# Performance work log

Measured on AMD Instinct MI355X. Metric: run time of the kernel, lower is better.

The kernel has to match this reference:

```python
import jax, jax.numpy as jnp
import numpy as np

R = 16
LORA_ALPHA = 32
SCALING = LORA_ALPHA / R  # use_rslora=False -> alpha/r = 2.0


def fwht(x):
    """Normalized fast Walsh-Hadamard transform along last axis (power-of-2 dim)."""
    n = x.shape[-1]
    batch = x.shape[:-1]
    h = 1
    while h < n:  # static loop, log2(n) iterations
        x = x.reshape(*batch, n // (2 * h), 2, h)
        a = x[..., 0, :]
        b = x[..., 1, :]
        x = jnp.stack([a + b, a - b], axis=-2).reshape(*batch, n)
        h *= 2
    return x * np.float32(1.0 / np.sqrt(n))


def quant_int8_ste(x):
    """Simulated symmetric per-row int8 quantization with straight-through estimator."""
    s = jnp.max(jnp.abs(x), axis=-1, keepdims=True) * np.float32(1.0 / 127.0)
    s = jnp.maximum(s, np.float32(1e-8))
    q = jnp.clip(jnp.round(x / s), -127.0, 127.0) * s
    return x + jax.lax.stop_gradient(q - x)


def setup_inputs() -> dict:
    key = jax.random.key(0)
    k1, k2, k3, k4 = jax.random.split(key, 4)
    B, S, D_in, D_out = 4, 2048, 4096, 4096
    x = jax.random.normal(k1, (B, S, D_in), dtype=jnp.float32)
    weight = jax.random.normal(k2, (D_out, D_in), dtype=jnp.float32) * np.float32(0.02)
    lora_A = jax.random.normal(k3, (R, D_in), dtype=jnp.float32) * np.float32(0.02)
    lora_B = jax.random.normal(k4, (D_out, R), dtype=jnp.float32) * np.float32(0.02)
    return {"x": x, "weight": weight, "lora_A": lora_A, "lora_B": lora_B}


def reference(x, weight, lora_A, lora_B):
    B, S, D_in = x.shape
    x2 = x.reshape(-1, D_in)  # [B*S, D_in]
    # Hadamard-rotate + quantize both operands (rotation is orthogonal, so
    # (xH)(WH)^T == xW^T up to quantization error) then GEMM.
    xq = quant_int8_ste(fwht(x2))          # [B*S, D_in]
    wq = quant_int8_ste(fwht(weight))      # [D_out, D_in]
    out = xq @ wq.T                        # [B*S, D_out]
    # LoRA side path (dropout p=0): B(A x) * scaling
    lora = (x2 @ lora_A.T) @ lora_B.T * np.float32(SCALING)
    return (out + lora).reshape(B, S, -1)
```

## Files before the change

### kernel.cpp

```cpp
#include <hip/hip_runtime.h>
#include <stdint.h>

typedef int v4i __attribute__((ext_vector_type(4)));

#define GLD_LDS16(gp, lp)                                                              \
  __builtin_amdgcn_global_load_lds((const __attribute__((address_space(1))) void*)(gp), \
                                   (__attribute__((address_space(3))) void*)(lp), 16, 0, 0)

__device__ __forceinline__ v4i lds_read_b128(uint32_t off) {
  v4i r;
  asm volatile("ds_read_b128 %0, %1" : "=v"(r) : "v"(off));
  return r;
}

__device__ __forceinline__ void fwht16(float v[16]) {
#pragma unroll
  for (int h = 1; h < 16; h <<= 1) {
#pragma unroll
    for (int i = 0; i < 16; ++i) {
      if (!(i & h)) {
        float a = v[i], b = v[i | h];
        v[i] = a + b;
        v[i | h] = a - b;
      }
    }
  }
}

__device__ __forceinline__ void fwht_row_load(const float* __restrict__ xr, int t,
                                              float v[16]) {
  const float4* p = reinterpret_cast<const float4*>(xr) + t * 4;
  float4 a = p[0], b = p[1], c = p[2], d = p[3];
  v[0] = a.x; v[1] = a.y; v[2] = a.z; v[3] = a.w;
  v[4] = b.x; v[5] = b.y; v[6] = b.z; v[7] = b.w;
  v[8] = c.x; v[9] = c.y; v[10] = c.z; v[11] = c.w;
  v[12] = d.x; v[13] = d.y; v[14] = d.z; v[15] = d.w;
}

__device__ __forceinline__ void fwht4096(float v[16], float* lds, int t) {
  fwht16(v);
#pragma unroll
  for (int e = 0; e < 16; ++e) {
    int idx = t * 16 + e;
    lds[idx + (idx >> 5)] = v[e];
  }
  __syncthreads();
#pragma unroll
  for (int e = 0; e < 16; ++e) {
    int idx = ((t >> 4) << 8) + (e << 4) + (t & 15);
    v[e] = lds[idx + (idx >> 5)];
  }
  fwht16(v);
#pragma unroll
  for (int e = 0; e < 16; ++e) {
    int idx = ((t >> 4) << 8) + (e << 4) + (t & 15);
    lds[idx + (idx >> 5)] = v[e];
  }
  __syncthreads();
#pragma unroll
  for (int e = 0; e < 16; ++e) {
    int idx = (e << 8) + t;
    v[e] = lds[idx + (idx >> 5)];
  }
  fwht16(v);
#pragma unroll
  for (int e = 0; e < 16; ++e) v[e] *= 0.015625f;
}

__global__ __launch_bounds__(256) void fwht_quant_kernel(const float* __restrict__ X,
                                                         int8_t* __restrict__ Q,
                                                         float* __restrict__ S) {
  const int row = blockIdx.x;
  const int t = threadIdx.x;
  __shared__ float lds[4224];
  __shared__ float wred[4];

  float v[16];
  fwht_row_load(X + (size_t)row * 4096, t, v);
  fwht4096(v, lds, t);

  float m = 0.f;
#pragma unroll
  for (int e = 0; e < 16; ++e) m = fmaxf(m, fabsf(v[e]));
#pragma unroll
  for (int off = 32; off > 0; off >>= 1) m = fmaxf(m, __shfl_xor(m, off));
  if ((t & 63) == 0) wred[t >> 6] = m;
  __syncthreads();
  m = fmaxf(fmaxf(wred[0], wred[1]), fmaxf(wred[2], wred[3]));
  const float s = fmaxf(m * (1.0f / 127.0f), 1e-8f);
  if (t == 0) S[row] = s;
  int8_t* qr = Q + (size_t)row * 4096;
#pragma unroll
  for (int e = 0; e < 16; ++e) {
    float q = rintf(v[e] / s);
    q = fminf(fmaxf(q, -127.f), 127.f);
    qr[(e << 8) + t] = (int8_t)(int)q;
  }
}

__global__ __launch_bounds__(256) void fwht_nq_kernel(const float* __restrict__ X,
                                                      float* __restrict__ F) {
  const int row = blockIdx.x;
  const int t = threadIdx.x;
  __shared__ float lds[4224];
  float v[16];
  fwht_row_load(X + (size_t)row * 4096, t, v);
  fwht4096(v, lds, t);
  float* fr = F + (size_t)row * 4096;
#pragma unroll
  for (int e = 0; e < 16; ++e) fr[(e << 8) + t] = v[e];
}

__global__ __launch_bounds__(256) void lora_t_partial_q(const int8_t* __restrict__ Qx,
                                                        const float* __restrict__ Sx,
                                                        const float* __restrict__ Ah,
                                                        float* __restrict__ tpart) {
  __shared__ float As[16][512];
  const int t = threadIdx.x;
  const int kc = blockIdx.y;
  const int row = blockIdx.x * 256 + t;
  for (int i = t; i < 2048; i += 256) {
    int r = i >> 7, c4 = i & 127;
    reinterpret_cast<float4*>(&As[r][0])[c4] =
        reinterpret_cast<const float4*>(Ah + (size_t)r * 4096 + kc * 512)[c4];
  }
  __syncthreads();
  float acc[16];
#pragma unroll
  for (int r = 0; r < 16; ++r) acc[r] = 0.f;
  const int8_t* xr = Qx + (size_t)row * 4096 + kc * 512;
  for (int k = 0; k < 512; k += 16) {
    int4 pv = *reinterpret_cast<const int4*>(xr + k);
    int us[4] = {pv.x, pv.y, pv.z, pv.w};
#pragma unroll
    for (int b = 0; b < 4; ++b) {
#pragma unroll
      for (int j = 0; j < 4; ++j) {
        float f = (float)((int)(int8_t)(us[b] >> (8 * j)));
        int kk = k + b * 4 + j;
#pragma unroll
        for (int r = 0; r < 16; ++r) acc[r] = fmaf(f, As[r][kk], acc[r]);
      }
    }
  }
  const float s = Sx[row];
  float* tp = tpart + ((size_t)kc * 8192 + row) * 16;
#pragma unroll
  for (int r = 0; r < 16; ++r) tp[r] = acc[r] * s;
}

__global__ __launch_bounds__(256) void lora_t_reduce_kernel(const float* __restrict__ tpart,
                                                            float* __restrict__ tmat) {
  int i = blockIdx.x * 256 + threadIdx.x;
  float s = 0.f;
#pragma unroll
  for (int kc = 0; kc < 8; ++kc) s += tpart[(size_t)kc * 131072 + i];
  tmat[i] = s;
}

__global__ __launch_bounds__(512, 2) void gemm_i8_kernel(
    const int8_t* __restrict__ Aq, const int8_t* __restrict__ Bq,
    const float* __restrict__ Sx, const float* __restrict__ Sw,
    const float* __restrict__ Tm, const float* __restrict__ LB,
    float* __restrict__ out) {
  __shared__ __align__(16) char smem[131072];

  const int tid = threadIdx.x;
  const int lane = tid & 63;
  const int w = tid >> 6;
  const int wm = w >> 2;
  const int wn = w & 3;

  int bid = (int)blockIdx.x;
  bid = (bid & 7) * 64 + (bid >> 3);
  const int bm = bid >> 4;
  const int bn = bid & 15;

  const int8_t* Ag = Aq + (size_t)bm * 256 * 4096;
  const int8_t* Bg = Bq + (size_t)bn * 256 * 4096;

  const uint32_t sbase = (uint32_t)(uintptr_t)(void*)smem;

  const size_t gA0 = (size_t)(w * 32 + (lane >> 2)) * 4096 +
                     (((lane & 3) ^ ((lane >> 3) & 3)) << 4);
  const size_t gA1 = gA0 + 16 * 4096;

#define STAGE_STEP(s)                                                   \
  do {                                                                  \
    char* dst = smem + ((s) & 3) * 32768 + w * 2048;                    \
    const size_t kb = (size_t)(s) << 6;                                 \
    GLD_LDS16(Ag + gA0 + kb, dst);                                      \
    GLD_LDS16(Ag + gA1 + kb, dst + 1024);                               \
    GLD_LDS16(Bg + gA0 + kb, dst + 16384);                              \
    GLD_LDS16(Bg + gA1 + kb, dst + 16384 + 1024);                       \
  } while (0)

  int aoff[8], boff[4];
#pragma unroll
  for (int mi = 0; mi < 8; ++mi) {
    int r = wm * 128 + mi * 16 + (lane & 15);
    aoff[mi] = r * 64 + ((((lane >> 4)) ^ ((r >> 1) & 3)) << 4);
  }
#pragma unroll
  for (int ni = 0; ni < 4; ++ni) {
    int r = wn * 64 + ni * 16 + (lane & 15);
    boff[ni] = 16384 + r * 64 + ((((lane >> 4)) ^ ((r >> 1) & 3)) << 4);
  }

  v4i acc[8][4];
#pragma unroll
  for (int i = 0; i < 8; ++i)
#pragma unroll
    for (int n = 0; n < 4; ++n) {
      v4i z = {0, 0, 0, 0};
      acc[i][n] = z;
    }

  STAGE_STEP(0);
  STAGE_STEP(1);
  STAGE_STEP(2);
  asm volatile("s_waitcnt vmcnt(8)" ::: "memory");
  __builtin_amdgcn_s_barrier();
  __builtin_amdgcn_sched_barrier(0);

#define MFMA16(MH)                                                                        \
  do {                                                                                    \
    __builtin_amdgcn_s_setprio(1);                                                        \
    _Pragma("unroll") for (int i = 0; i < 4; ++i) _Pragma("unroll") for (int n = 0;       \
                                                                        n < 4; ++n)       \
        acc[(MH)*4 + i][n] =                                                              \
        __builtin_amdgcn_mfma_i32_16x16x64_i8(af[i], bf[n], acc[(MH)*4 + i][n], 0, 0, 0); \
    __builtin_amdgcn_s_setprio(0);                                                        \
  } while (0)

#pragma unroll 1
  for (int t = 0; t < 64; ++t) {
    const uint32_t bufR = sbase + (t & 3) * 32768;
    if (t <= 60) STAGE_STEP(t + 3);

    v4i af[4], bf[4], af2[4];
#pragma unroll
    for (int n = 0; n < 4; ++n) bf[n] = lds_read_b128(bufR + boff[n]);
#pragma unroll
    for (int i = 0; i < 4; ++i) af[i] = lds_read_b128(bufR + aoff[i]);
#pragma unroll
    for (int i = 0; i < 4; ++i) af2[i] = lds_read_b128(bufR + aoff[4 + i]);
    asm volatile("s_waitcnt lgkmcnt(4)" ::: "memory");
    __builtin_amdgcn_sched_barrier(0);
    MFMA16(0);
#pragma unroll
    for (int i = 0; i < 4; ++i) af[i] = af2[i];
    asm volatile("s_waitcnt lgkmcnt(0)" ::: "memory");
    __builtin_amdgcn_sched_barrier(0);
    MFMA16(1);

    if (t <= 60)
      asm volatile("s_waitcnt vmcnt(8)" ::: "memory");
    else if (t == 61)
      asm volatile("s_waitcnt vmcnt(4)" ::: "memory");
    else if (t == 62)
      asm volatile("s_waitcnt vmcnt(0)" ::: "memory");
    if (t < 63) {
      __builtin_amdgcn_s_barrier();
      __builtin_amdgcn_sched_barrier(0);
    }
  }

  __syncthreads();
  float* tl = (float*)smem;
  float* bl = (float*)(smem + 17408);
  for (int i = tid; i < 1024; i += 512) {
    int r = i >> 2, q4 = (i & 3) * 4;
    float4 tv = *reinterpret_cast<const float4*>(Tm + (size_t)(bm * 256 + r) * 16 + q4);
    tl[r * 17 + q4 + 0] = tv.x;
    tl[r * 17 + q4 + 1] = tv.y;
    tl[r * 17 + q4 + 2] = tv.z;
    tl[r * 17 + q4 + 3] = tv.w;
    float4 bv = *reinterpret_cast<const float4*>(LB + (size_t)(bn * 256 + r) * 16 + q4);
    bl[r * 17 + q4 + 0] = bv.x;
    bl[r * 17 + q4 + 1] = bv.y;
    bl[r * 17 + q4 + 2] = bv.z;
    bl[r * 17 + q4 + 3] = bv.w;
  }
  __syncthreads();

  float blv[4][16], swv[4];
#pragma unroll
  for (int ni = 0; ni < 4; ++ni) {
    int cl = wn * 64 + ni * 16 + (lane & 15);
    swv[ni] = Sw[bn * 256 + cl];
#pragma unroll
    for (int q = 0; q < 16; ++q) blv[ni][q] = bl[cl * 17 + q];
  }
#pragma unroll
  for (int mi = 0; mi < 8; ++mi) {
#pragma unroll
    for (int rr = 0; rr < 4; ++rr) {
      int rl = wm * 128 + mi * 16 + (lane >> 4) * 4 + rr;
      float sxv = Sx[bm * 256 + rl];
      float tv[16];
#pragma unroll
      for (int q = 0; q < 16; ++q) tv[q] = tl[rl * 17 + q];
      float* orow = out + (size_t)(bm * 256 + rl) * 4096 + bn * 256;
#pragma unroll
      for (int ni = 0; ni < 4; ++ni) {
        float dot = 0.f;
#pragma unroll
        for (int q = 0; q < 16; ++q) dot = fmaf(tv[q], blv[ni][q], dot);
        int cl = wn * 64 + ni * 16 + (lane & 15);
        orow[cl] = sxv * swv[ni] * (float)acc[mi][ni][rr] + 2.0f * dot;
      }
    }
  }
}

extern "C" void kernel_launch(void* const* d_in, const int* in_sizes, int n_in,
                              void* d_out, int out_size, void* d_ws, size_t ws_size,
                              hipStream_t stream) {
  const float* x = (const float*)d_in[0];
  const float* wgt = (const float*)d_in[1];
  const float* lA = (const float*)d_in[2];
  const float* lB = (const float*)d_in[3];
  float* out = (float*)d_out;

  char* ws = (char*)d_ws;
  int8_t* qx = (int8_t*)ws;
  int8_t* qw = (int8_t*)(ws + 33554432);
  float* sx = (float*)(ws + 50331648);
  float* sw = (float*)(ws + 50364416);
  float* tmat = (float*)(ws + 50380800);
  float* tpart = (float*)(ws + 50905088);
  float* Ah = (float*)(ws + 55099392);

  fwht_quant_kernel<<<8192, 256, 0, stream>>>(x, qx, sx);
  fwht_quant_kernel<<<4096, 256, 0, stream>>>(wgt, qw, sw);
  fwht_nq_kernel<<<16, 256, 0, stream>>>(lA, Ah);
  lora_t_partial_q<<<dim3(32, 8), 256, 0, stream>>>(qx, sx, Ah, tpart);
  lora_t_reduce_kernel<<<512, 256, 0, stream>>>(tpart, tmat);
  gemm_i8_kernel<<<512, 512, 0, stream>>>(qx, qw, sx, sw, tmat, lB, out);
}
```

Before: 277.2 us.

## Retile int8 GEMM to 256x128 blocks with 32x32 MFMA and triple buffering

Reshapes the int8 GEMM block tile from 256x256 to 256x128 and doubles the grid to 1024 blocks. The inner product moves from 16x16x64 to 32x32x32 int8 MFMA instructions, and the LDS pipeline drops from four stages to three rotating buffers. The goal is lower LDS use (72KB), so launch bounds can allow more blocks per CU and raise occupancy. The trade-off is less reuse of each loaded A tile, since every A row block is now fetched for twice as many column blocks.

New measurement: 299.3 us. +8.0%, slower.

```diff
diff --git a/kernel.cpp b/kernel.cpp
--- a/kernel.cpp
+++ b/kernel.cpp
@@ -2,6 +2,7 @@
 #include <stdint.h>
 
 typedef int v4i __attribute__((ext_vector_type(4)));
+typedef int v16i __attribute__((ext_vector_type(16)));
 
 #define GLD_LDS16(gp, lp)                                                              \
   __builtin_amdgcn_global_load_lds((const __attribute__((address_space(1))) void*)(gp), \
@@ -158,112 +159,125 @@
   tmat[i] = s;
 }
 
-__global__ __launch_bounds__(512, 2) void gemm_i8_kernel(
+__global__ __launch_bounds__(512, 4) void gemm_i8_kernel(
     const int8_t* __restrict__ Aq, const int8_t* __restrict__ Bq,
     const float* __restrict__ Sx, const float* __restrict__ Sw,
     const float* __restrict__ Tm, const float* __restrict__ LB,
     float* __restrict__ out) {
-  __shared__ __align__(16) char smem[131072];
+  __shared__ __align__(16) char smem[73728];
 
   const int tid = threadIdx.x;
   const int lane = tid & 63;
   const int w = tid >> 6;
-  const int wm = w >> 2;
-  const int wn = w & 3;
+  const int wm = w >> 1;
+  const int wn = w & 1;
 
   int bid = (int)blockIdx.x;
-  bid = (bid & 7) * 64 + (bid >> 3);
-  const int bm = bid >> 4;
-  const int bn = bid & 15;
+  bid = (bid & 7) * 128 + (bid >> 3);
+  const int bm = bid >> 5;
+  const int bn = bid & 31;
 
   const int8_t* Ag = Aq + (size_t)bm * 256 * 4096;
-  const int8_t* Bg = Bq + (size_t)bn * 256 * 4096;
+  const int8_t* Bg = Bq + (size_t)bn * 128 * 4096;
 
   const uint32_t sbase = (uint32_t)(uintptr_t)(void*)smem;
 
-  const size_t gA0 = (size_t)(w * 32 + (lane >> 2)) * 4096 +
-                     (((lane & 3) ^ ((lane >> 3) & 3)) << 4);
-  const size_t gA1 = gA0 + 16 * 4096;
-
-#define STAGE_STEP(s)                                                   \
-  do {                                                                  \
-    char* dst = smem + ((s) & 3) * 32768 + w * 2048;                    \
-    const size_t kb = (size_t)(s) << 6;                                 \
-    GLD_LDS16(Ag + gA0 + kb, dst);                                      \
-    GLD_LDS16(Ag + gA1 + kb, dst + 1024);                               \
-    GLD_LDS16(Bg + gA0 + kb, dst + 16384);                              \
-    GLD_LDS16(Bg + gA1 + kb, dst + 16384 + 1024);                       \
+  const uint32_t srcOff = (uint32_t)(((lane & 3) ^ ((lane >> 3) & 3)) << 4);
+  const uint32_t gA0 = (uint32_t)((w * 32 + (lane >> 2)) * 4096) + srcOff;
+  const uint32_t gA1 = gA0 + 16 * 4096;
+  const uint32_t gB0 = (uint32_t)((w * 16 + (lane >> 2)) * 4096) + srcOff;
+
+#define STAGE_STEP(s, bufbase)                                           \
+  do {                                                                   \
+    const uint32_t kb = (uint32_t)(s) << 6;                              \
+    GLD_LDS16(Ag + kb + gA0, smem + (bufbase) + w * 2048);               \
+    GLD_LDS16(Ag + kb + gA1, smem + (bufbase) + w * 2048 + 1024);        \
+    GLD_LDS16(Bg + kb + gB0, smem + (bufbase) + 16384 + w * 1024);       \
   } while (0)
 
-  int aoff[8], boff[4];
-#pragma unroll
-  for (int mi = 0; mi < 8; ++mi) {
-    int r = wm * 128 + mi * 16 + (lane & 15);
-    aoff[mi] = r * 64 + ((((lane >> 4)) ^ ((r >> 1) & 3)) << 4);
-  }
-#pragma unroll
-  for (int ni = 0; ni < 4; ++ni) {
-    int r = wn * 64 + ni * 16 + (lane & 15);
-    boff[ni] = 16384 + r * 64 + ((((lane >> 4)) ^ ((r >> 1) & 3)) << 4);
-  }
-
-  v4i acc[8][4];
-#pragma unroll
-  for (int i = 0; i < 8; ++i)
-#pragma unroll
-    for (int n = 0; n < 4; ++n) {
-      v4i z = {0, 0, 0, 0};
+  int aoff[2][2], boff[2][2];
+  const int swz = (lane >> 1) & 3;
+  const int khalf = lane >> 5;
+#pragma unroll
+  for (int mt = 0; mt < 2; ++mt) {
+    int r = wm * 64 + mt * 32 + (lane & 31);
+#pragma unroll
+    for (int ks = 0; ks < 2; ++ks) {
+      int c = ((ks << 1) | khalf) ^ swz;
+      aoff[mt][ks] = r * 64 + (c << 4);
+    }
+  }
+#pragma unroll
+  for (int nt = 0; nt < 2; ++nt) {
+    int r = wn * 64 + nt * 32 + (lane & 31);
+#pragma unroll
+    for (int ks = 0; ks < 2; ++ks) {
+      int c = ((ks << 1) | khalf) ^ swz;
+      boff[nt][ks] = 16384 + r * 64 + (c << 4);
+    }
+  }
+
+  v16i acc[2][2];
+#pragma unroll
+  for (int i = 0; i < 2; ++i)
+#pragma unroll
+    for (int n = 0; n < 2; ++n) {
+      v16i z = {0};
       acc[i][n] = z;
     }
 
-  STAGE_STEP(0);
-  STAGE_STEP(1);
-  STAGE_STEP(2);
-  asm volatile("s_waitcnt vmcnt(8)" ::: "memory");
+  STAGE_STEP(0, 0);
+  STAGE_STEP(1, 24576);
+  asm volatile("s_waitcnt vmcnt(3)" ::: "memory");
   __builtin_amdgcn_s_barrier();
   __builtin_amdgcn_sched_barrier(0);
 
-#define MFMA16(MH)                                                                        \
-  do {                                                                                    \
-    __builtin_amdgcn_s_setprio(1);                                                        \
-    _Pragma("unroll") for (int i = 0; i < 4; ++i) _Pragma("unroll") for (int n = 0;       \
-                                                                        n < 4; ++n)       \
-        acc[(MH)*4 + i][n] =                                                              \
-        __builtin_amdgcn_mfma_i32_16x16x64_i8(af[i], bf[n], acc[(MH)*4 + i][n], 0, 0, 0); \
-    __builtin_amdgcn_s_setprio(0);                                                        \
-  } while (0)
+  uint32_t bc = 0, bn1 = 24576, bn2 = 49152;
 
 #pragma unroll 1
   for (int t = 0; t < 64; ++t) {
-    const uint32_t bufR = sbase + (t & 3) * 32768;
-    if (t <= 60) STAGE_STEP(t + 3);
-
-    v4i af[4], bf[4], af2[4];
-#pragma unroll
-    for (int n = 0; n < 4; ++n) bf[n] = lds_read_b128(bufR + boff[n]);
-#pragma unroll
-    for (int i = 0; i < 4; ++i) af[i] = lds_read_b128(bufR + aoff[i]);
-#pragma unroll
-    for (int i = 0; i < 4; ++i) af2[i] = lds_read_b128(bufR + aoff[4 + i]);
+    if (t <= 61) STAGE_STEP(t + 2, bn2);
+
+    const uint32_t R = sbase + bc;
+    v4i a0[2], b0[2], a1[2], b1[2];
+    b0[0] = lds_read_b128(R + boff[0][0]);
+    b0[1] = lds_read_b128(R + boff[1][0]);
+    a0[0] = lds_read_b128(R + aoff[0][0]);
+    a0[1] = lds_read_b128(R + aoff[1][0]);
+    b1[0] = lds_read_b128(R + boff[0][1]);
+    b1[1] = lds_read_b128(R + boff[1][1]);
+    a1[0] = lds_read_b128(R + aoff[0][1]);
+    a1[1] = lds_read_b128(R + aoff[1][1]);
+
     asm volatile("s_waitcnt lgkmcnt(4)" ::: "memory");
     __builtin_amdgcn_sched_barrier(0);
-    MFMA16(0);
-#pragma unroll
-    for (int i = 0; i < 4; ++i) af[i] = af2[i];
+    __builtin_amdgcn_s_setprio(1);
+    acc[0][0] = __builtin_amdgcn_mfma_i32_32x32x32_i8(a0[0], b0[0], acc[0][0], 0, 0, 0);
+    acc[0][1] = __builtin_amdgcn_mfma_i32_32x32x32_i8(a0[0], b0[1], acc[0][1], 0, 0, 0);
+    acc[1][0] = __builtin_amdgcn_mfma_i32_32x32x32_i8(a0[1], b0[0], acc[1][0], 0, 0, 0);
+    acc[1][1] = __builtin_amdgcn_mfma_i32_32x32x32_i8(a0[1], b0[1], acc[1][1], 0, 0, 0);
+    __builtin_amdgcn_s_setprio(0);
+
     asm volatile("s_waitcnt lgkmcnt(0)" ::: "memory");
     __builtin_amdgcn_sched_barrier(0);
-    MFMA16(1);
-
-    if (t <= 60)
-      asm volatile("s_waitcnt vmcnt(8)" ::: "memory");
-    else if (t == 61)
-      asm volatile("s_waitcnt vmcnt(4)" ::: "memory");
+    __builtin_amdgcn_s_setprio(1);
+    acc[0][0] = __builtin_amdgcn_mfma_i32_32x32x32_i8(a1[0], b1[0], acc[0][0], 0, 0, 0);
+    acc[0][1] = __builtin_amdgcn_mfma_i32_32x32x32_i8(a1[0], b1[1], acc[0][1], 0, 0, 0);
+    acc[1][0] = __builtin_amdgcn_mfma_i32_32x32x32_i8(a1[1], b1[0], acc[1][0], 0, 0, 0);
+    acc[1][1] = __builtin_amdgcn_mfma_i32_32x32x32_i8(a1[1], b1[1], acc[1][1], 0, 0, 0);
+    __builtin_amdgcn_s_setprio(0);
+
+    if (t <= 61)
+      asm volatile("s_waitcnt vmcnt(3)" ::: "memory");
     else if (t == 62)
       asm volatile("s_waitcnt vmcnt(0)" ::: "memory");
-    if (t < 63) {
-      __builtin_amdgcn_s_barrier();
-      __builtin_amdgcn_sched_barrier(0);
-    }
+    __builtin_amdgcn_s_barrier();
+    __builtin_amdgcn_sched_barrier(0);
+
+    uint32_t tmp = bc;
+    bc = bn1;
+    bn1 = bn2;
+    bn2 = tmp;
   }
 
   __syncthreads();
@@ -276,7 +290,10 @@
     tl[r * 17 + q4 + 1] = tv.y;
     tl[r * 17 + q4 + 2] = tv.z;
     tl[r * 17 + q4 + 3] = tv.w;
-    float4 bv = *reinterpret_cast<const float4*>(LB + (size_t)(bn * 256 + r) * 16 + q4);
+  }
+  for (int i = tid; i < 512; i += 512) {
+    int r = i >> 2, q4 = (i & 3) * 4;
+    float4 bv = *reinterpret_cast<const float4*>(LB + (size_t)(bn * 128 + r) * 16 + q4);
     bl[r * 17 + q4 + 0] = bv.x;
     bl[r * 17 + q4 + 1] = bv.y;
     bl[r * 17 + q4 + 2] = bv.z;
@@ -284,31 +301,31 @@
   }
   __syncthreads();
 
-  float blv[4][16], swv[4];
-#pragma unroll
-  for (int ni = 0; ni < 4; ++ni) {
-    int cl = wn * 64 + ni * 16 + (lane & 15);
-    swv[ni] = Sw[bn * 256 + cl];
-#pragma unroll
-    for (int q = 0; q < 16; ++q) blv[ni][q] = bl[cl * 17 + q];
-  }
-#pragma unroll
-  for (int mi = 0; mi < 8; ++mi) {
-#pragma unroll
-    for (int rr = 0; rr < 4; ++rr) {
-      int rl = wm * 128 + mi * 16 + (lane >> 4) * 4 + rr;
+  float blv[2][16], swv[2];
+#pragma unroll
+  for (int nt = 0; nt < 2; ++nt) {
+    int cl = wn * 64 + nt * 32 + (lane & 31);
+    swv[nt] = Sw[bn * 128 + cl];
+#pragma unroll
+    for (int q = 0; q < 16; ++q) blv[nt][q] = bl[cl * 17 + q];
+  }
+#pragma unroll
+  for (int mt = 0; mt < 2; ++mt) {
+#pragma unroll
+    for (int rg = 0; rg < 16; ++rg) {
+      int rl = wm * 64 + mt * 32 + (rg & 3) + 8 * (rg >> 2) + 4 * (lane >> 5);
       float sxv = Sx[bm * 256 + rl];
       float tv[16];
 #pragma unroll
       for (int q = 0; q < 16; ++q) tv[q] = tl[rl * 17 + q];
-      float* orow = out + (size_t)(bm * 256 + rl) * 4096 + bn * 256;
-#pragma unroll
-      for (int ni = 0; ni < 4; ++ni) {
+      float* orow = out + (size_t)(bm * 256 + rl) * 4096 + bn * 128;
+#pragma unroll
+      for (int nt = 0; nt < 2; ++nt) {
         float dot = 0.f;
 #pragma unroll
-        for (int q = 0; q < 16; ++q) dot = fmaf(tv[q], blv[ni][q], dot);
-        int cl = wn * 64 + ni * 16 + (lane & 15);
-        orow[cl] = sxv * swv[ni] * (float)acc[mi][ni][rr] + 2.0f * dot;
+        for (int q = 0; q < 16; ++q) dot = fmaf(tv[q], blv[nt][q], dot);
+        int cl = wn * 64 + nt * 32 + (lane & 31);
+        orow[cl] = sxv * swv[nt] * (float)acc[mt][nt][rg] + 2.0f * dot;
       }
     }
   }
@@ -337,5 +354,5 @@
   fwht_nq_kernel<<<16, 256, 0, stream>>>(lA, Ah);
   lora_t_partial_q<<<dim3(32, 8), 256, 0, stream>>>(qx, sx, Ah, tpart);
   lora_t_reduce_kernel<<<512, 256, 0, stream>>>(tpart, tmat);
-  gemm_i8_kernel<<<512, 512, 0, stream>>>(qx, qw, sx, sw, tmat, lB, out);
-}
+  gemm_i8_kernel<<<1024, 512, 0, stream>>>(qx, qw, sx, sw, tmat, lB, out);
+}
```

## Software-pipeline LDS fragment reads across K steps and pack int8 quant stores

Applied to the files above, without the earlier changes.

The int8 GEMM main loop now prefetches the next stage's A and B fragments from LDS while the second half of the current stage's MFMAs runs, so LDS read latency overlaps tensor-core work instead of stalling before each MFMA group. The quantize kernel stages int8 results through LDS and writes 16-byte packed stores instead of scattered byte stores. Global address arithmetic switches from 64-bit to 32-bit offsets. The cost is more live fragment registers, which may pressure occupancy.

Result: slower. 307.6 us (+11.0%).

```diff
diff --git a/kernel.cpp b/kernel.cpp
--- a/kernel.cpp
+++ b/kernel.cpp
@@ -72,7 +72,7 @@
                                                          float* __restrict__ S) {
   const int row = blockIdx.x;
   const int t = threadIdx.x;
-  __shared__ float lds[4224];
+  __shared__ __align__(16) float lds[4224];
   __shared__ float wred[4];
 
   float v[16];
@@ -89,20 +89,26 @@
   m = fmaxf(fmaxf(wred[0], wred[1]), fmaxf(wred[2], wred[3]));
   const float s = fmaxf(m * (1.0f / 127.0f), 1e-8f);
   if (t == 0) S[row] = s;
-  int8_t* qr = Q + (size_t)row * 4096;
+
+  __syncthreads();
+  char* b8 = (char*)lds;
 #pragma unroll
   for (int e = 0; e < 16; ++e) {
     float q = rintf(v[e] / s);
     q = fminf(fmaxf(q, -127.f), 127.f);
-    qr[(e << 8) + t] = (int8_t)(int)q;
-  }
+    int idx = (e << 8) + t;
+    b8[idx + ((idx >> 8) << 4)] = (char)(int)q;
+  }
+  __syncthreads();
+  int4 pack = *reinterpret_cast<const int4*>(b8 + t * 16 + ((t >> 4) << 4));
+  reinterpret_cast<int4*>(Q + (size_t)row * 4096)[t] = pack;
 }
 
 __global__ __launch_bounds__(256) void fwht_nq_kernel(const float* __restrict__ X,
                                                       float* __restrict__ F) {
   const int row = blockIdx.x;
   const int t = threadIdx.x;
-  __shared__ float lds[4224];
+  __shared__ __align__(16) float lds[4224];
   float v[16];
   fwht_row_load(X + (size_t)row * 4096, t, v);
   fwht4096(v, lds, t);
@@ -181,30 +187,31 @@
 
   const uint32_t sbase = (uint32_t)(uintptr_t)(void*)smem;
 
-  const size_t gA0 = (size_t)(w * 32 + (lane >> 2)) * 4096 +
-                     (((lane & 3) ^ ((lane >> 3) & 3)) << 4);
-  const size_t gA1 = gA0 + 16 * 4096;
+  const uint32_t srcOff = (uint32_t)(((lane & 3) ^ ((lane >> 3) & 3)) << 4);
+  const uint32_t gR0 = (uint32_t)((w * 32 + (lane >> 2)) * 4096) + srcOff;
+  const uint32_t gR1 = gR0 + 16 * 4096;
 
 #define STAGE_STEP(s)                                                   \
   do {                                                                  \
     char* dst = smem + ((s) & 3) * 32768 + w * 2048;                    \
-    const size_t kb = (size_t)(s) << 6;                                 \
-    GLD_LDS16(Ag + gA0 + kb, dst);                                      \
-    GLD_LDS16(Ag + gA1 + kb, dst + 1024);                               \
-    GLD_LDS16(Bg + gA0 + kb, dst + 16384);                              \
-    GLD_LDS16(Bg + gA1 + kb, dst + 16384 + 1024);                       \
+    const uint32_t kb = (uint32_t)(s) << 6;                             \
+    GLD_LDS16(Ag + gR0 + kb, dst);                                      \
+    GLD_LDS16(Ag + gR1 + kb, dst + 1024);                               \
+    GLD_LDS16(Bg + gR0 + kb, dst + 16384);                              \
+    GLD_LDS16(Bg + gR1 + kb, dst + 16384 + 1024);                       \
   } while (0)
 
   int aoff[8], boff[4];
+  const int cc = lane >> 4;
 #pragma unroll
   for (int mi = 0; mi < 8; ++mi) {
     int r = wm * 128 + mi * 16 + (lane & 15);
-    aoff[mi] = r * 64 + ((((lane >> 4)) ^ ((r >> 1) & 3)) << 4);
+    aoff[mi] = r * 64 + ((cc ^ ((r >> 1) & 3)) << 4);
   }
 #pragma unroll
   for (int ni = 0; ni < 4; ++ni) {
     int r = wn * 64 + ni * 16 + (lane & 15);
-    boff[ni] = 16384 + r * 64 + ((((lane >> 4)) ^ ((r >> 1) & 3)) << 4);
+    boff[ni] = 16384 + r * 64 + ((cc ^ ((r >> 1) & 3)) << 4);
   }
 
   v4i acc[8][4];
@@ -223,36 +230,34 @@
   __builtin_amdgcn_s_barrier();
   __builtin_amdgcn_sched_barrier(0);
 
-#define MFMA16(MH)                                                                        \
-  do {                                                                                    \
-    __builtin_amdgcn_s_setprio(1);                                                        \
-    _Pragma("unroll") for (int i = 0; i < 4; ++i) _Pragma("unroll") for (int n = 0;       \
-                                                                        n < 4; ++n)       \
-        acc[(MH)*4 + i][n] =                                                              \
-        __builtin_amdgcn_mfma_i32_16x16x64_i8(af[i], bf[n], acc[(MH)*4 + i][n], 0, 0, 0); \
-    __builtin_amdgcn_s_setprio(0);                                                        \
-  } while (0)
+  v4i ap[4], bc[4];
+#pragma unroll
+  for (int n = 0; n < 4; ++n) bc[n] = lds_read_b128(sbase + boff[n]);
+#pragma unroll
+  for (int i = 0; i < 4; ++i) ap[i] = lds_read_b128(sbase + aoff[i]);
+  asm volatile("s_waitcnt lgkmcnt(0)" ::: "memory");
+  __builtin_amdgcn_sched_barrier(0);
 
 #pragma unroll 1
   for (int t = 0; t < 64; ++t) {
-    const uint32_t bufR = sbase + (t & 3) * 32768;
+    const uint32_t R = sbase + (t & 3) * 32768;
+    const uint32_t Rn = sbase + ((t + 1) & 3) * 32768;
     if (t <= 60) STAGE_STEP(t + 3);
 
-    v4i af[4], bf[4], af2[4];
-#pragma unroll
-    for (int n = 0; n < 4; ++n) bf[n] = lds_read_b128(bufR + boff[n]);
-#pragma unroll
-    for (int i = 0; i < 4; ++i) af[i] = lds_read_b128(bufR + aoff[i]);
-#pragma unroll
-    for (int i = 0; i < 4; ++i) af2[i] = lds_read_b128(bufR + aoff[4 + i]);
-    asm volatile("s_waitcnt lgkmcnt(4)" ::: "memory");
-    __builtin_amdgcn_sched_barrier(0);
-    MFMA16(0);
-#pragma unroll
-    for (int i = 0; i < 4; ++i) af[i] = af2[i];
+    v4i af2[4];
+#pragma unroll
+    for (int i = 0; i < 4; ++i) af2[i] = lds_read_b128(R + aoff[4 + i]);
+
+    __builtin_amdgcn_s_setprio(1);
+#pragma unroll
+    for (int i = 0; i < 4; ++i)
+#pragma unroll
+      for (int n = 0; n < 4; ++n)
+        acc[i][n] = __builtin_amdgcn_mfma_i32_16x16x64_i8(ap[i], bc[n], acc[i][n], 0, 0, 0);
+    __builtin_amdgcn_s_setprio(0);
+
     asm volatile("s_waitcnt lgkmcnt(0)" ::: "memory");
     __builtin_amdgcn_sched_barrier(0);
-    MFMA16(1);
 
     if (t <= 60)
       asm volatile("s_waitcnt vmcnt(8)" ::: "memory");
@@ -263,6 +268,34 @@
     if (t < 63) {
       __builtin_amdgcn_s_barrier();
       __builtin_amdgcn_sched_barrier(0);
+      v4i bn_[4];
+#pragma unroll
+      for (int n = 0; n < 4; ++n) bn_[n] = lds_read_b128(Rn + boff[n]);
+#pragma unroll
+      for (int i = 0; i < 4; ++i) ap[i] = lds_read_b128(Rn + aoff[i]);
+
+      __builtin_amdgcn_s_setprio(1);
+#pragma unroll
+      for (int i = 0; i < 4; ++i)
+#pragma unroll
+        for (int n = 0; n < 4; ++n)
+          acc[4 + i][n] =
+              __builtin_amdgcn_mfma_i32_16x16x64_i8(af2[i], bc[n], acc[4 + i][n], 0, 0, 0);
+      __builtin_amdgcn_s_setprio(0);
+
+      asm volatile("s_waitcnt lgkmcnt(0)" ::: "memory");
+      __builtin_amdgcn_sched_barrier(0);
+#pragma unroll
+      for (int n = 0; n < 4; ++n) bc[n] = bn_[n];
+    } else {
+      __builtin_amdgcn_s_setprio(1);
+#pragma unroll
+      for (int i = 0; i < 4; ++i)
+#pragma unroll
+        for (int n = 0; n < 4; ++n)
+          acc[4 + i][n] =
+              __builtin_amdgcn_mfma_i32_16x16x64_i8(af2[i], bc[n], acc[4 + i][n], 0, 0, 0);
+      __builtin_amdgcn_s_setprio(0);
     }
   }
 
```
